# Kernel tuning notes

Hardware: AMD Instinct MI355X
Metric: run time of the kernel (lower is better)

## Reference

```python
import jax, jax.numpy as jnp
import numpy as np

B, L = 32768, 2048
MARGIN = 0.1

def setup_inputs() -> dict:
    key = jax.random.key(0)
    k1, k2, k3 = jax.random.split(key, 3)
    scores = jax.random.normal(k1, (B, L), dtype=jnp.float32)
    # ragged candidate lengths in [0, L]; zeros are skipped samples
    candidate_lengths = jax.random.randint(k2, (B,), 0, L + 1, dtype=jnp.int32).astype(jnp.int64)
    # at most one positive per row: a random index; it only lands inside the
    # valid region for some rows, naturally mixing pos/no-pos samples
    pos_idx = jax.random.randint(k3, (B,), 0, L, dtype=jnp.int32)
    labels = (jnp.arange(L, dtype=jnp.int32)[None, :] == pos_idx[:, None]).astype(jnp.int64)
    return {"scores": scores, "candidate_lengths": candidate_lengths, "labels": labels}

def reference(scores, candidate_lengths, labels):
    B_, L_ = scores.shape
    valid = jnp.arange(L_)[None, :] < candidate_lengths[:, None]          # [B, L]
    pos_mask = (labels == 1) & valid
    neg_mask = (labels == 0) & valid
    has_pos = jnp.any(pos_mask, axis=-1)                                   # label.sum() > 0
    has_neg = jnp.any(neg_mask, axis=-1)
    # single positive score per row (0 if none), then the -margin fallback
    pos_score = jnp.sum(jnp.where(pos_mask, scores, 0.0), axis=-1)         # [B]
    chosen = jnp.where(has_pos, pos_score, -MARGIN)                        # [B]
    hinge = jnp.maximum(MARGIN + scores - chosen[:, None], 0.0)           # [B, L]
    neg_cnt = jnp.sum(neg_mask, axis=-1)
    per_sample = jnp.sum(jnp.where(neg_mask, hinge, 0.0), axis=-1) / jnp.maximum(neg_cnt, 1).astype(scores.dtype)
    valid_obs = (candidate_lengths > 0) & has_neg
    n_valid = jnp.sum(valid_obs).astype(scores.dtype)
    total = jnp.sum(jnp.where(valid_obs, per_sample, 0.0))
    return jnp.where(n_valid > 0, total / jnp.maximum(n_valid, 1.0), 0.0)
```

## Files before the change

kernel.cpp:

```cpp
#include <hip/hip_runtime.h>


constexpr int L_DIM = 2048;
constexpr float MARGIN = 0.1f;
constexpr int NBUCKET = 1024;

__global__ __launch_bounds__(256) void hinge_row_kernel(
    const float* __restrict__ scores,
    const int*   __restrict__ lens,
    const int*   __restrict__ labels,
    float* __restrict__ acc_sum,
    float* __restrict__ acc_cnt)
{
    const int row = blockIdx.x;
    int len = lens[row];
    if (len <= 0) return;
    if (len > L_DIM) len = L_DIM;

    const int t = threadIdx.x;
    const size_t base = (size_t)row * L_DIM;
    const float4* s4 = reinterpret_cast<const float4*>(scores + base);
    const int4*   l4 = reinterpret_cast<const int4*>(labels + base);

    float sc[8];
    unsigned negmask = 0;
    float pos_local = 0.f;
    float haspos_local = 0.f;

    #pragma unroll
    for (int k = 0; k < 2; ++k) {
        const int v = t + k * 256;
        const int j = v * 4;
        if (j < len) {
            const float4 sv = s4[v];
            const int4   lv = l4[v];
            const float se[4] = {sv.x, sv.y, sv.z, sv.w};
            const int    le[4] = {lv.x, lv.y, lv.z, lv.w};
            #pragma unroll
            for (int e = 0; e < 4; ++e) {
                const int jj = j + e;
                if (jj < len) {
                    if (le[e] == 1) { pos_local += se[e]; haspos_local = 1.f; }
                    else            { sc[k * 4 + e] = se[e];
                                      negmask |= 1u << (k * 4 + e); }
                }
            }
        }
    }

    float a = pos_local, b = haspos_local;
    #pragma unroll
    for (int off = 32; off > 0; off >>= 1) {
        a += __shfl_down(a, off, 64);
        b += __shfl_down(b, off, 64);
    }
    __shared__ float red_a[4], red_b[4];
    const int wave = t >> 6;
    const int lane = t & 63;
    if (lane == 0) { red_a[wave] = a; red_b[wave] = b; }
    __syncthreads();
    const float pos_score = red_a[0] + red_a[1] + red_a[2] + red_a[3];
    const float has_pos   = red_b[0] + red_b[1] + red_b[2] + red_b[3];

    const float chosen = (has_pos > 0.f) ? pos_score : -MARGIN;

    float hsum = 0.f, hcnt = 0.f;
    #pragma unroll
    for (int i = 0; i < 8; ++i) {
        if (negmask & (1u << i)) {
            hsum += fmaxf(MARGIN + sc[i] - chosen, 0.f);
            hcnt += 1.f;
        }
    }
    #pragma unroll
    for (int off = 32; off > 0; off >>= 1) {
        hsum += __shfl_down(hsum, off, 64);
        hcnt += __shfl_down(hcnt, off, 64);
    }
    __shared__ float red_h[4], red_c[4];
    if (lane == 0) { red_h[wave] = hsum; red_c[wave] = hcnt; }
    __syncthreads();
    if (t == 0) {
        const float H = red_h[0] + red_h[1] + red_h[2] + red_h[3];
        const float C = red_c[0] + red_c[1] + red_c[2] + red_c[3];
        if (C > 0.f) {
            atomicAdd(&acc_sum[row & (NBUCKET - 1)], H / C);
            atomicAdd(&acc_cnt[row & (NBUCKET - 1)], 1.f);
        }
    }
}

__global__ __launch_bounds__(1024) void finalize_kernel(
    const float* __restrict__ acc_sum,
    const float* __restrict__ acc_cnt,
    float* __restrict__ out)
{
    const int t = threadIdx.x;
    float s = acc_sum[t];
    float c = acc_cnt[t];
    #pragma unroll
    for (int off = 32; off > 0; off >>= 1) {
        s += __shfl_down(s, off, 64);
        c += __shfl_down(c, off, 64);
    }
    __shared__ float sh_s[16], sh_c[16];
    const int wave = t >> 6, lane = t & 63;
    if (lane == 0) { sh_s[wave] = s; sh_c[wave] = c; }
    __syncthreads();
    if (t == 0) {
        float S = 0.f, C = 0.f;
        #pragma unroll
        for (int i = 0; i < 16; ++i) { S += sh_s[i]; C += sh_c[i]; }
        out[0] = (C > 0.f) ? (S / C) : 0.f;
    }
}

extern "C" void kernel_launch(void* const* d_in, const int* in_sizes, int n_in,
                              void* d_out, int out_size, void* d_ws, size_t ws_size,
                              hipStream_t stream) {
    const float* scores = (const float*)d_in[0];
    const int*   lens   = (const int*)d_in[1];
    const int*   labels = (const int*)d_in[2];
    const int B = in_sizes[1];

    float* acc_sum = (float*)d_ws;
    float* acc_cnt = acc_sum + NBUCKET;

    hipMemsetAsync(d_ws, 0, 2 * NBUCKET * sizeof(float), stream);

    hinge_row_kernel<<<B, 256, 0, stream>>>(scores, lens, labels, acc_sum, acc_cnt);
    finalize_kernel<<<1, NBUCKET, 0, stream>>>(acc_sum, acc_cnt, (float*)d_out);
}
```

Baseline: 456.9 us.

## Map one row per wavefront with a persistent grid and accumulate per wave

Replaces the one-row-per-256-thread-block mapping with one row per 64-lane wavefront, looping persistently over rows in a capped grid. Reductions become wave-local xor shuffles, so the shared-memory exchanges and __syncthreads are gone, and each wave does a single atomic at the end instead of one per row. Invalid slots are filled with a large negative sentinel so the hinge loop needs no mask, and the negative count is derived as len minus positives. In exchange each lane holds 32 scores in registers and issues 8 vector loads per row, which raises register pressure and may cut occupancy; rows of different lengths can also leave waves unevenly loaded.

Result: slower. 467.5 us (+2.3%).

```diff
diff --git a/kernel.cpp b/kernel.cpp
--- a/kernel.cpp
+++ b/kernel.cpp
@@ -4,89 +4,89 @@
 constexpr int L_DIM = 2048;
 constexpr float MARGIN = 0.1f;
 constexpr int NBUCKET = 1024;
+constexpr int ROWS_PER_BLOCK = 4;
+constexpr int MAX_BLOCKS = 2048;
+
+typedef float f4 __attribute__((ext_vector_type(4)));
+typedef int   i4 __attribute__((ext_vector_type(4)));
 
 __global__ __launch_bounds__(256) void hinge_row_kernel(
     const float* __restrict__ scores,
     const int*   __restrict__ lens,
     const int*   __restrict__ labels,
     float* __restrict__ acc_sum,
-    float* __restrict__ acc_cnt)
+    float* __restrict__ acc_cnt,
+    int B)
 {
-    const int row = blockIdx.x;
-    int len = lens[row];
-    if (len <= 0) return;
-    if (len > L_DIM) len = L_DIM;
+    const int t    = threadIdx.x;
+    const int wave = t >> 6;
+    const int lane = t & 63;
+    const int wid     = blockIdx.x * ROWS_PER_BLOCK + wave;
+    const int wstride = gridDim.x * ROWS_PER_BLOCK;
 
-    const int t = threadIdx.x;
-    const size_t base = (size_t)row * L_DIM;
-    const float4* s4 = reinterpret_cast<const float4*>(scores + base);
-    const int4*   l4 = reinterpret_cast<const int4*>(labels + base);
+    float wsum = 0.f;
+    float wcnt = 0.f;
 
-    float sc[8];
-    unsigned negmask = 0;
-    float pos_local = 0.f;
-    float haspos_local = 0.f;
+    for (int row = wid; row < B; row += wstride) {
+        int len = lens[row];
+        if (len <= 0) continue;
+        if (len > L_DIM) len = L_DIM;
 
-    #pragma unroll
-    for (int k = 0; k < 2; ++k) {
-        const int v = t + k * 256;
-        const int j = v * 4;
-        if (j < len) {
-            const float4 sv = s4[v];
-            const int4   lv = l4[v];
-            const float se[4] = {sv.x, sv.y, sv.z, sv.w};
-            const int    le[4] = {lv.x, lv.y, lv.z, lv.w};
+        const size_t base = (size_t)row * L_DIM;
+        const f4* s4 = reinterpret_cast<const f4*>(scores + base);
+        const i4* l4 = reinterpret_cast<const i4*>(labels + base);
+        const int vmax = (len - 1) >> 2;
+
+        float sc[32];
+        float pos_local  = 0.f;
+        float npos_local = 0.f;
+
+        #pragma unroll
+        for (int k = 0; k < 8; ++k) {
             #pragma unroll
-            for (int e = 0; e < 4; ++e) {
-                const int jj = j + e;
-                if (jj < len) {
-                    if (le[e] == 1) { pos_local += se[e]; haspos_local = 1.f; }
-                    else            { sc[k * 4 + e] = se[e];
-                                      negmask |= 1u << (k * 4 + e); }
+            for (int e = 0; e < 4; ++e) sc[4 * k + e] = -1e30f;
+            if ((k << 8) < len) {
+                const int v  = lane + (k << 6);
+                const int vc = (v < vmax) ? v : vmax;
+                const f4 sv = s4[vc];
+                const i4 lv = l4[vc];
+                #pragma unroll
+                for (int e = 0; e < 4; ++e) {
+                    const int  jj    = (v << 2) + e;
+                    const bool valid = jj < len;
+                    const bool isp   = valid && (lv[e] == 1);
+                    if (isp) { pos_local += sv[e]; npos_local += 1.f; }
+                    if (valid && !isp) sc[4 * k + e] = sv[e];
                 }
             }
         }
+
+        float p = pos_local, np = npos_local;
+        #pragma unroll
+        for (int off = 1; off < 64; off <<= 1) {
+            p  += __shfl_xor(p,  off, 64);
+            np += __shfl_xor(np, off, 64);
+        }
+        const float chosen = (np > 0.f) ? p : -MARGIN;
+
+        float h = 0.f;
+        #pragma unroll
+        for (int i = 0; i < 32; ++i)
+            h += fmaxf(MARGIN + sc[i] - chosen, 0.f);
+        #pragma unroll
+        for (int off = 1; off < 64; off <<= 1)
+            h += __shfl_xor(h, off, 64);
+
+        const float negc = (float)len - np;
+        if (negc > 0.f) {
+            wsum += h / negc;
+            wcnt += 1.f;
+        }
     }
 
-    float a = pos_local, b = haspos_local;
-    #pragma unroll
-    for (int off = 32; off > 0; off >>= 1) {
-        a += __shfl_down(a, off, 64);
-        b += __shfl_down(b, off, 64);
-    }
-    __shared__ float red_a[4], red_b[4];
-    const int wave = t >> 6;
-    const int lane = t & 63;
-    if (lane == 0) { red_a[wave] = a; red_b[wave] = b; }
-    __syncthreads();
-    const float pos_score = red_a[0] + red_a[1] + red_a[2] + red_a[3];
-    const float has_pos   = red_b[0] + red_b[1] + red_b[2] + red_b[3];
-
-    const float chosen = (has_pos > 0.f) ? pos_score : -MARGIN;
-
-    float hsum = 0.f, hcnt = 0.f;
-    #pragma unroll
-    for (int i = 0; i < 8; ++i) {
-        if (negmask & (1u << i)) {
-            hsum += fmaxf(MARGIN + sc[i] - chosen, 0.f);
-            hcnt += 1.f;
-        }
-    }
-    #pragma unroll
-    for (int off = 32; off > 0; off >>= 1) {
-        hsum += __shfl_down(hsum, off, 64);
-        hcnt += __shfl_down(hcnt, off, 64);
-    }
-    __shared__ float red_h[4], red_c[4];
-    if (lane == 0) { red_h[wave] = hsum; red_c[wave] = hcnt; }
-    __syncthreads();
-    if (t == 0) {
-        const float H = red_h[0] + red_h[1] + red_h[2] + red_h[3];
-        const float C = red_c[0] + red_c[1] + red_c[2] + red_c[3];
-        if (C > 0.f) {
-            atomicAdd(&acc_sum[row & (NBUCKET - 1)], H / C);
-            atomicAdd(&acc_cnt[row & (NBUCKET - 1)], 1.f);
-        }
+    if (lane == 0 && wcnt > 0.f) {
+        atomicAdd(&acc_sum[wid & (NBUCKET - 1)], wsum);
+        atomicAdd(&acc_cnt[wid & (NBUCKET - 1)], wcnt);
     }
 }
 
@@ -128,6 +128,9 @@
 
     hipMemsetAsync(d_ws, 0, 2 * NBUCKET * sizeof(float), stream);
 
-    hinge_row_kernel<<<B, 256, 0, stream>>>(scores, lens, labels, acc_sum, acc_cnt);
+    int nblocks = (B + ROWS_PER_BLOCK - 1) / ROWS_PER_BLOCK;
+    if (nblocks > MAX_BLOCKS) nblocks = MAX_BLOCKS;
+    hinge_row_kernel<<<nblocks, 256, 0, stream>>>(scores, lens, labels,
+                                                  acc_sum, acc_cnt, B);
     finalize_kernel<<<1, NBUCKET, 0, stream>>>(acc_sum, acc_cnt, (float*)d_out);
 }
```
